# Kernel optimization log

Hardware: AMD Instinct MI355X
Metric: run time of the kernel (lower is better)

## Reference

```python
import jax, jax.numpy as jnp
import numpy as np

V, E, H, L, S, B, FE = 50257, 768, 12, 4, 1024, 2, 4
HD = E // H
EPS = 1e-5


def setup_inputs() -> dict:
    key = jax.random.key(0)
    ks = jax.random.split(key, 16)
    def n(k, shape, scale=0.02):
        return jax.random.normal(k, shape, jnp.float32) * scale
    x = jax.random.randint(ks[0], (B, S), 0, V)
    mask = jnp.tril(jnp.ones((S, S), jnp.int32))[None, None]  # (1,1,S,S) causal
    return {
        "x": x,
        "mask": mask,
        "embed_W": n(ks[1], (V, E)),
        "pos_embed": n(ks[2], (1, S, E)),
        "fc_out_W": n(ks[3], (L, E, E)),
        "fc_out_b": jnp.zeros((L, E), jnp.float32),
        "gate_W": n(ks[4], (L, E, E)),
        "gate_b": jnp.zeros((L, E), jnp.float32),
        "ln1_g": jnp.ones((L, E), jnp.float32),
        "ln1_b": jnp.zeros((L, E), jnp.float32),
        "ln2_g": jnp.ones((L, E), jnp.float32),
        "ln2_b": jnp.zeros((L, E), jnp.float32),
        "ff1_W": n(ks[5], (L, E, FE * E)),
        "ff1_b": jnp.zeros((L, FE * E), jnp.float32),
        "ff2_W": n(ks[6], (L, FE * E, E)),
        "ff2_b": jnp.zeros((L, E), jnp.float32),
        "lnf_g": jnp.ones((E,), jnp.float32),
        "lnf_b": jnp.zeros((E,), jnp.float32),
        "head_W": n(ks[7], (E, V)),
    }


def _layernorm(y, g, b):
    m = jnp.mean(y, -1, keepdims=True)
    v = jnp.mean((y - m) ** 2, -1, keepdims=True)
    return (y - m) * jax.lax.rsqrt(v + EPS) * g + b


def reference(x, mask, embed_W, pos_embed, fc_out_W, fc_out_b, gate_W, gate_b,
              ln1_g, ln1_b, ln2_g, ln2_b, ff1_W, ff1_b, ff2_W, ff2_b,
              lnf_g, lnf_b, head_W):
    h = embed_W[x] + pos_embed[:, :x.shape[1], :]  # (B,S,E)
    scale = 1.0 / np.sqrt(HD)
    for i in range(L):
        # NOTE: source never applies the q/k/v Linear layers; heads are split directly.
        q = h.reshape(B, S, H, HD).transpose(0, 2, 1, 3)  # (B,H,S,HD)
        energy = jnp.einsum('bhqd,bhkd->bhqk', q, q)
        energy = jnp.where(mask == 0, jnp.float32(-1e20), energy)
        attn = jax.nn.softmax(energy * scale, axis=-1)
        o = jnp.einsum('bhqk,bhkd->bhqd', attn, q)
        o = o.transpose(0, 2, 1, 3).reshape(B, S, E)
        o = o @ fc_out_W[i] + fc_out_b[i]
        gate = jax.nn.sigmoid(jnp.mean(h, 1, keepdims=True) @ gate_W[i] + gate_b[i])
        h = _layernorm(gate * o + h, ln1_g[i], ln1_b[i])
        ff = jax.nn.gelu(h @ ff1_W[i] + ff1_b[i], approximate=False) @ ff2_W[i] + ff2_b[i]
        h = _layernorm(ff + h, ln2_g[i], ln2_b[i])
    h = _layernorm(h, lnf_g, lnf_b)
    logits = h @ head_W  # (B,S,V)
    return logits
```

## Files before the change

kernel.cpp:

```cpp
#include <hip/hip_runtime.h>
#include <hip/hip_bf16.h>

#define V 50257
#define E 768
#define NH 12
#define NL 4
#define SS 1024
#define BB 2
#define FEE 4
#define HD 64
#define EPSL 1e-5f
#define NPADH 50432

typedef __hip_bfloat16 bf16;
typedef __attribute__((ext_vector_type(8))) short short8;
typedef __attribute__((ext_vector_type(4))) float f32x4;

#define GLD_SRC(p) (const __attribute__((address_space(1))) void*)(p)
#define GLD_DST(p) (__attribute__((address_space(3))) void*)(p)

__global__ __launch_bounds__(256) void embed_kernel(const int* __restrict__ x, const float* __restrict__ eW,
                                                    const float* __restrict__ pos, float* __restrict__ h){
  size_t i = (size_t)blockIdx.x*256 + threadIdx.x;
  if (i >= (size_t)BB*SS*E) return;
  int e = (int)(i % E);
  size_t bs = i / E;
  int s = (int)(bs % SS);
  int tok = x[bs];
  h[i] = eW[(size_t)tok*E + e] + pos[(size_t)s*E + e];
}

__global__ __launch_bounds__(256) void cvt_attn(const float* __restrict__ h, bf16* __restrict__ hb,
                                                bf16* __restrict__ vT){
  __shared__ float t[64][65];
  int bid = blockIdx.x;
  int st = bid & 15, hh = (bid >> 4) % NH, b = bid / (16*NH);
  int s0 = st*64;
  int c = threadIdx.x & 63, rr = threadIdx.x >> 6;
  #pragma unroll
  for (int i = 0; i < 16; ++i){
    int r = rr*16 + i;
    float v = h[(size_t)(b*SS + s0 + r)*E + hh*HD + c];
    hb[(size_t)(b*SS + s0 + r)*E + hh*HD + c] = __float2bfloat16(v);
    t[r][c] = v;
  }
  __syncthreads();
  #pragma unroll
  for (int i = 0; i < 16; ++i){
    int d = rr*16 + i;
    vT[(size_t)((b*NH + hh)*HD + d)*SS + s0 + c] = __float2bfloat16(t[c][d]);
  }
}

__global__ __launch_bounds__(256) void attn_mfma(const bf16* __restrict__ hb, const bf16* __restrict__ vT,
                                                 bf16* __restrict__ Ab){
  __shared__ short Qs[64*64];
  __shared__ short Ks[128*64];
  __shared__ short Vs[64*128];
  __shared__ short Ps[4][16*128];
  int tid = threadIdx.x, wave = tid >> 6, lane = tid & 63;
  int bid = blockIdx.x;
  int qt = 15 - (bid & 15);
  int hh = (bid >> 4) % NH, b = bid / (16*NH);
  int q0 = qt*64;
  int l15 = lane & 15, l4 = lane >> 4;
  int sw7 = l15 & 7;

  #pragma unroll
  for (int rnd = 0; rnd < 2; ++rnd){
    int o = rnd*256 + tid; int row = o >> 3; int cs = (((o & 7) ^ (row & 7))*8);
    __builtin_amdgcn_global_load_lds(GLD_SRC(hb + ((size_t)(b*SS + q0 + row)*E + hh*HD + cs)),
                                     GLD_DST(Qs + o*8), 16, 0, 0);
  }

  float mrun[4], lrun[4];
  #pragma unroll
  for (int j = 0; j < 4; ++j){ mrun[j] = -1e30f; lrun[j] = 0.f; }
  f32x4 acco[4] = {};

  int nkt = (qt >> 1) + 1;
  for (int kt = 0; kt < nkt; ++kt){
    int k0 = kt*128;
    __syncthreads();
    #pragma unroll
    for (int rnd = 0; rnd < 4; ++rnd){
      int o = rnd*256 + tid; int row = o >> 3; int cs = (((o & 7) ^ (row & 7))*8);
      __builtin_amdgcn_global_load_lds(GLD_SRC(hb + ((size_t)(b*SS + k0 + row)*E + hh*HD + cs)),
                                       GLD_DST(Ks + o*8), 16, 0, 0);
    }
    #pragma unroll
    for (int rnd = 0; rnd < 4; ++rnd){
      int o = rnd*256 + tid; int row = o >> 4; int cs = (((o & 15) ^ (row & 15))*8);
      __builtin_amdgcn_global_load_lds(GLD_SRC(vT + ((size_t)((b*NH + hh)*HD + row)*SS + k0 + cs)),
                                       GLD_DST(Vs + o*8), 16, 0, 0);
    }
    __syncthreads();

    f32x4 s[8] = {};
    __builtin_amdgcn_s_setprio(1);
    #pragma unroll
    for (int kk = 0; kk < 2; ++kk){
      int slot = kk*4 + l4;
      short8 af = *(const short8*)&Qs[(wave*16 + l15)*64 + ((slot ^ sw7)*8)];
      #pragma unroll
      for (int n = 0; n < 8; ++n){
        short8 bf8 = *(const short8*)&Ks[(n*16 + l15)*64 + ((slot ^ sw7)*8)];
        s[n] = __builtin_amdgcn_mfma_f32_16x16x32_bf16(af, bf8, s[n], 0, 0, 0);
      }
    }
    __builtin_amdgcn_s_setprio(0);

    bool diag = (kt == nkt - 1);
    #pragma unroll
    for (int j = 0; j < 4; ++j){
      int qg = q0 + wave*16 + l4*4 + j;
      float tmax = -1e30f;
      #pragma unroll
      for (int n = 0; n < 8; ++n){
        float v = s[n][j]*0.125f;
        if (diag && (k0 + n*16 + l15) > qg) v = -1e30f;
        s[n][j] = v; tmax = fmaxf(tmax, v);
      }
      tmax = fmaxf(tmax, __shfl_xor(tmax, 1, 64));
      tmax = fmaxf(tmax, __shfl_xor(tmax, 2, 64));
      tmax = fmaxf(tmax, __shfl_xor(tmax, 4, 64));
      tmax = fmaxf(tmax, __shfl_xor(tmax, 8, 64));
      float mnew = fmaxf(mrun[j], tmax);
      float alpha = __expf(mrun[j] - mnew);
      float rsum = 0.f;
      #pragma unroll
      for (int n = 0; n < 8; ++n){
        float p = __expf(s[n][j] - mnew);
        s[n][j] = p; rsum += p;
      }
      rsum += __shfl_xor(rsum, 1, 64);
      rsum += __shfl_xor(rsum, 2, 64);
      rsum += __shfl_xor(rsum, 4, 64);
      rsum += __shfl_xor(rsum, 8, 64);
      lrun[j] = lrun[j]*alpha + rsum;
      mrun[j] = mnew;
      #pragma unroll
      for (int n = 0; n < 4; ++n) acco[n][j] *= alpha;
      int prow = l4*4 + j;
      #pragma unroll
      for (int n = 0; n < 8; ++n){
        bf16 hv = __float2bfloat16(s[n][j]);
        int slot = (n*2 + (l15 >> 3)) ^ prow;
        Ps[wave][prow*128 + slot*8 + (l15 & 7)] = __builtin_bit_cast(short, hv);
      }
    }
    __syncthreads();

    __builtin_amdgcn_s_setprio(1);
    #pragma unroll
    for (int kk = 0; kk < 4; ++kk){
      int slot = kk*4 + l4;
      short8 pa = *(const short8*)&Ps[wave][l15*128 + ((slot ^ l15)*8)];
      #pragma unroll
      for (int n = 0; n < 4; ++n){
        short8 vb = *(const short8*)&Vs[(n*16 + l15)*128 + ((slot ^ l15)*8)];
        acco[n] = __builtin_amdgcn_mfma_f32_16x16x32_bf16(pa, vb, acco[n], 0, 0, 0);
      }
    }
    __builtin_amdgcn_s_setprio(0);
  }

  #pragma unroll
  for (int j = 0; j < 4; ++j){
    float inv = 1.f / lrun[j];
    int qg = q0 + wave*16 + l4*4 + j;
    #pragma unroll
    for (int n = 0; n < 4; ++n){
      Ab[(size_t)(b*SS + qg)*E + hh*HD + n*16 + l15] = __float2bfloat16(acco[n][j]*inv);
    }
  }
}

__global__ __launch_bounds__(256) void hmean1_kernel(const float* __restrict__ h, float* __restrict__ ph){
  int bid = blockIdx.x;
  int ec = bid % 3, tc = (bid/3) & 15, b = bid / 48;
  int e = ec*256 + threadIdx.x;
  float s = 0.f;
  #pragma unroll 8
  for (int t = tc*64; t < tc*64 + 64; ++t) s += h[((size_t)b*SS + t)*E + e];
  ph[((size_t)b*16 + tc)*E + e] = s;
}

__global__ __launch_bounds__(256) void gate1_kernel(const float* __restrict__ ph, const float* __restrict__ gW,
                                                    float* __restrict__ pg){
  int bid = blockIdx.x;
  int ec = bid % 3, kc = (bid/3) & 3, b = bid / 12;
  int nn = ec*256 + threadIdx.x;
  __shared__ float hms[192];
  if (threadIdx.x < 192){
    int k = kc*192 + threadIdx.x;
    float s = 0.f;
    #pragma unroll
    for (int tc = 0; tc < 16; ++tc) s += ph[((size_t)b*16 + tc)*E + k];
    hms[threadIdx.x] = s * (1.0f/SS);
  }
  __syncthreads();
  float acc = 0.f;
  #pragma unroll 8
  for (int j = 0; j < 192; ++j) acc += hms[j] * gW[(size_t)(kc*192 + j)*E + nn];
  pg[((size_t)b*4 + kc)*E + nn] = acc;
}

__global__ __launch_bounds__(256) void wcvt_kernel(const float* __restrict__ W, bf16* __restrict__ Wt,
                                                   int K, int N, int Npad){
  int l = blockIdx.z;
  W  += (size_t)l*K*N;
  Wt += (size_t)l*Npad*K;
  __shared__ float t[32][33];
  int n0 = blockIdx.x*32, k0 = blockIdx.y*32;
  int tx = threadIdx.x & 31, ty8 = threadIdx.x >> 5;
  #pragma unroll
  for (int i = 0; i < 4; ++i){
    int k = k0 + ty8 + i*8, n = n0 + tx;
    t[ty8 + i*8][tx] = (k < K && n < N) ? W[(size_t)k*N + n] : 0.f;
  }
  __syncthreads();
  #pragma unroll
  for (int i = 0; i < 4; ++i){
    int n = n0 + ty8 + i*8, k = k0 + tx;
    if (n < Npad && k < K) Wt[(size_t)n*K + k] = __float2bfloat16(t[tx][ty8 + i*8]);
  }
}

template<int EPI>
__global__ __launch_bounds__(256) void mfma_gemm(const bf16* __restrict__ A, const bf16* __restrict__ Bt,
                                                 const float* __restrict__ bias, void* __restrict__ Cv,
                                                 int M, int N, int Kslice, int Ktot){
  __shared__ short As[2][128*64];
  __shared__ short Bs[2][128*64];
  int tid = threadIdx.x;
  int wave = tid >> 6, lane = tid & 63;
  int wr = wave >> 1, wc = wave & 1;
  int l15 = lane & 15, l4 = lane >> 4;
  int sw7 = l15 & 7;
  int n0 = blockIdx.x * 128, m0 = blockIdx.y * 128;
  size_t koff = (size_t)blockIdx.z * Kslice;
  f32x4 acc[4][4] = {};
  int srow = tid >> 3;
  int sj = tid & 7;
  const int nks = Kslice >> 6;

  #define STAGE128(bsel, kt) do {                                              \
    int kb = (kt)*64;                                                          \
    _Pragma("unroll")                                                          \
    for (int iss = 0; iss < 4; ++iss){                                         \
      int r = srow + iss*32;                                                   \
      int cs = ((sj ^ (r & 7))*8);                                             \
      __builtin_amdgcn_global_load_lds(GLD_SRC(A + (size_t)(m0 + r)*Ktot + koff + kb + cs),  \
                                       GLD_DST(&As[bsel][r*64 + sj*8]), 16, 0, 0);           \
      __builtin_amdgcn_global_load_lds(GLD_SRC(Bt + (size_t)(n0 + r)*Ktot + koff + kb + cs), \
                                       GLD_DST(&Bs[bsel][r*64 + sj*8]), 16, 0, 0);           \
    }                                                                          \
  } while(0)

  STAGE128(0, 0);
  __syncthreads();
  for (int kt = 0; kt < nks; ++kt){
    int cur = kt & 1;
    if (kt + 1 < nks) STAGE128(cur ^ 1, kt + 1);
    __builtin_amdgcn_s_setprio(1);
    #pragma unroll
    for (int kk = 0; kk < 2; ++kk){
      int slot = kk*4 + l4;
      short8 af[4], bfr[4];
      #pragma unroll
      for (int m = 0; m < 4; ++m)
        af[m] = *(const short8*)&As[cur][(wr*64 + m*16 + l15)*64 + ((slot ^ sw7)*8)];
      #pragma unroll
      for (int n = 0; n < 4; ++n)
        bfr[n] = *(const short8*)&Bs[cur][(wc*64 + n*16 + l15)*64 + ((slot ^ sw7)*8)];
      #pragma unroll
      for (int m = 0; m < 4; ++m)
        #pragma unroll
        for (int n = 0; n < 4; ++n)
          acc[m][n] = __builtin_amdgcn_mfma_f32_16x16x32_bf16(af[m], bfr[n], acc[m][n], 0, 0, 0);
    }
    __builtin_amdgcn_s_setprio(0);
    __syncthreads();
  }
  #undef STAGE128

  float* Cf = (float*)Cv + (size_t)blockIdx.z * M * N;
  int lrow = l4*4;
  #pragma unroll
  for (int m = 0; m < 4; ++m){
    int row = m0 + wr*64 + m*16 + lrow;
    #pragma unroll
    for (int n = 0; n < 4; ++n){
      int col = n0 + wc*64 + n*16 + l15;
      if (col >= N) continue;
      #pragma unroll
      for (int j = 0; j < 4; ++j){
        float v = acc[m][n][j];
        if (EPI == 3){
          v += bias[col];
          v = 0.5f*v*(1.0f + erff(v*0.70710678f));
          ((bf16*)Cv)[(size_t)(row + j)*N + col] = __float2bfloat16(v);
        } else {
          Cf[(size_t)(row + j)*N + col] = v;
        }
      }
    }
  }
}

__global__ __launch_bounds__(512, 2) void gemm256(const bf16* __restrict__ A, const bf16* __restrict__ Bt,
                                                  float* __restrict__ C, int M, int N, int K, int MT){
  __shared__ short As[2][256*64];
  __shared__ short Bs[2][256*64];
  int tid = threadIdx.x;
  int wave = tid >> 6, lane = tid & 63;
  int wr = wave >> 2, wc = wave & 3;
  int l15 = lane & 15, l4 = lane >> 4;
  int sw7 = l15 & 7;

  int lid = blockIdx.x;
  int cpx = gridDim.x >> 3;
  int wg = (lid & 7)*cpx + (lid >> 3);
  int m0 = (wg % MT)*256, n0 = (wg / MT)*256;

  int srow = tid >> 3;
  int sj = tid & 7;
  const int nks = K >> 6;

  #define STAGE256(bsel, kt) do {                                             \
    int kb = (kt)*64;                                                         \
    _Pragma("unroll")                                                         \
    for (int rnd = 0; rnd < 4; ++rnd){                                        \
      int r = rnd*64 + srow;                                                  \
      int cs = ((sj ^ (r & 7))*8);                                            \
      __builtin_amdgcn_global_load_lds(GLD_SRC(A + (size_t)(m0 + r)*K + kb + cs),   \
                                       GLD_DST(&As[bsel][r*64 + sj*8]), 16, 0, 0);  \
      __builtin_amdgcn_global_load_lds(GLD_SRC(Bt + (size_t)(n0 + r)*K + kb + cs),  \
                                       GLD_DST(&Bs[bsel][r*64 + sj*8]), 16, 0, 0);  \
    }                                                                         \
  } while(0)

  f32x4 acc[8][4] = {};
  STAGE256(0, 0);
  __syncthreads();
  for (int kt = 0; kt < nks; ++kt){
    int cur = kt & 1;
    if (kt + 1 < nks) STAGE256(cur ^ 1, kt + 1);
    __builtin_amdgcn_s_setprio(1);
    #pragma unroll
    for (int kk = 0; kk < 2; ++kk){
      int slot = kk*4 + l4;
      short8 af[8], bfr[4];
      #pragma unroll
      for (int m = 0; m < 8; ++m)
        af[m] = *(const short8*)&As[cur][(wr*128 + m*16 + l15)*64 + ((slot ^ sw7)*8)];
      #pragma unroll
      for (int n = 0; n < 4; ++n)
        bfr[n] = *(const short8*)&Bs[cur][(wc*64 + n*16 + l15)*64 + ((slot ^ sw7)*8)];
      #pragma unroll
      for (int m = 0; m < 8; ++m)
        #pragma unroll
        for (int n = 0; n < 4; ++n)
          acc[m][n] = __builtin_amdgcn_mfma_f32_16x16x32_bf16(af[m], bfr[n], acc[m][n], 0, 0, 0);
    }
    __builtin_amdgcn_s_setprio(0);
    __syncthreads();
  }
  #undef STAGE256

  int lrow = l4*4;
  #pragma unroll
  for (int m = 0; m < 8; ++m){
    int row = m0 + wr*128 + m*16 + lrow;
    #pragma unroll
    for (int n = 0; n < 4; ++n){
      int col = n0 + wc*64 + n*16 + l15;
      if (col >= N) continue;
      #pragma unroll
      for (int j = 0; j < 4; ++j)
        C[(size_t)(row + j)*N + col] = acc[m][n][j];
    }
  }
}

__global__ __launch_bounds__(256) void ln_kernel(const float* __restrict__ parts, int np,
                                                 const float* __restrict__ bias,
                                                 const float* __restrict__ resid,
                                                 const float* __restrict__ pg, const float* __restrict__ gb,
                                                 const float* __restrict__ g, const float* __restrict__ bta,
                                                 float* __restrict__ out, bf16* __restrict__ outb){
  const size_t PS = (size_t)BB*SS*E;
  int row = blockIdx.x;
  int b = row >> 10;
  int tid = threadIdx.x;
  __shared__ float sred[4];
  float y[3];
  float lsum = 0.f;
  #pragma unroll
  for (int i = 0; i < 3; ++i){
    int e = tid + i*256;
    float v = bias ? bias[e] : 0.f;
    for (int p = 0; p < np; ++p) v += parts[(size_t)p*PS + (size_t)row*E + e];
    if (pg){
      float ga = pg[(size_t)(b*4+0)*E + e] + pg[(size_t)(b*4+1)*E + e]
               + pg[(size_t)(b*4+2)*E + e] + pg[(size_t)(b*4+3)*E + e] + gb[e];
      v *= 1.0f / (1.0f + __expf(-ga));
    }
    if (resid) v += resid[(size_t)row*E + e];
    y[i] = v; lsum += v;
  }
  for (int off = 32; off > 0; off >>= 1) lsum += __shfl_down(lsum, off, 64);
  int wid = tid >> 6, lane = tid & 63;
  if (lane == 0) sred[wid] = lsum;
  __syncthreads();
  float mean = (sred[0]+sred[1]+sred[2]+sred[3]) * (1.0f/E);
  __syncthreads();
  float lvar = 0.f;
  #pragma unroll
  for (int i = 0; i < 3; ++i){ float d = y[i]-mean; lvar += d*d; }
  for (int off = 32; off > 0; off >>= 1) lvar += __shfl_down(lvar, off, 64);
  if (lane == 0) sred[wid] = lvar;
  __syncthreads();
  float rstd = rsqrtf((sred[0]+sred[1]+sred[2]+sred[3]) * (1.0f/E) + EPSL);
  __syncthreads();
  #pragma unroll
  for (int i = 0; i < 3; ++i){
    int e = tid + i*256;
    float r = (y[i]-mean)*rstd*g[e] + bta[e];
    out[(size_t)row*E + e] = r;
    if (outb) outb[(size_t)row*E + e] = __float2bfloat16(r);
  }
}

extern "C" void kernel_launch(void* const* d_in, const int* in_sizes, int n_in,
                              void* d_out, int out_size, void* d_ws, size_t ws_size,
                              hipStream_t stream) {
  const int*   x      = (const int*)  d_in[0];
  const float* embedW = (const float*)d_in[2];
  const float* pos    = (const float*)d_in[3];
  const float* fcW    = (const float*)d_in[4];
  const float* fcB    = (const float*)d_in[5];
  const float* gW     = (const float*)d_in[6];
  const float* gB     = (const float*)d_in[7];
  const float* ln1g   = (const float*)d_in[8];
  const float* ln1b   = (const float*)d_in[9];
  const float* ln2g   = (const float*)d_in[10];
  const float* ln2b   = (const float*)d_in[11];
  const float* f1W    = (const float*)d_in[12];
  const float* f1B    = (const float*)d_in[13];
  const float* f2W    = (const float*)d_in[14];
  const float* f2B    = (const float*)d_in[15];
  const float* lnfg   = (const float*)d_in[16];
  const float* lnfb   = (const float*)d_in[17];
  const float* headW  = (const float*)d_in[18];
  float* out = (float*)d_out;

  const size_t BSE = (size_t)BB*SS*E;
  float* h    = (float*)d_ws;
  float* o    = h   + BSE;
  float* tmp  = o   + BSE;
  float* ph   = tmp + 2*BSE;
  float* pg   = ph  + (size_t)BB*16*E;
  bf16* abA   = (bf16*)(pg + (size_t)BB*4*E);
  bf16* abF   = abA + BSE;
  bf16* WfcT  = abF + BSE*FEE;
  bf16* Wf1T  = WfcT + (size_t)NL*E*E;
  bf16* Wf2T  = Wf1T + (size_t)NL*FEE*E*E;
  bf16* WheadT= Wf2T + (size_t)NL*FEE*E*E;
  bf16* hb    = (bf16*)o;
  bf16* vT    = hb + BSE;

  const int rows = BB*SS;

  embed_kernel<<<(int)((BSE + 255)/256), 256, 0, stream>>>(x, embedW, pos, h);

  { dim3 g(E/32, E/32, NL);        wcvt_kernel<<<g, 256, 0, stream>>>(fcW, WfcT, E, E, E); }
  { dim3 g((FEE*E)/32, E/32, NL);  wcvt_kernel<<<g, 256, 0, stream>>>(f1W, Wf1T, E, FEE*E, FEE*E); }
  { dim3 g(E/32, (FEE*E)/32, NL);  wcvt_kernel<<<g, 256, 0, stream>>>(f2W, Wf2T, FEE*E, E, E); }
  { dim3 g(NPADH/32, E/32, 1);     wcvt_kernel<<<g, 256, 0, stream>>>(headW, WheadT, E, V, NPADH); }

  for (int l = 0; l < NL; ++l){
    size_t oEE = (size_t)l*E*E, oE = (size_t)l*E, oFb = (size_t)l*FEE*E;

    hmean1_kernel<<<BB*16*3, 256, 0, stream>>>(h, ph);
    gate1_kernel<<<BB*4*3, 256, 0, stream>>>(ph, gW + oEE, pg);

    cvt_attn<<<BB*NH*16, 256, 0, stream>>>(h, hb, vT);
    attn_mfma<<<BB*NH*16, 256, 0, stream>>>(hb, vT, abA);

    { dim3 g(E/128, rows/128, 2);
      mfma_gemm<0><<<g, 256, 0, stream>>>(abA, WfcT + oEE, nullptr, tmp, rows, E, E/2, E); }

    ln_kernel<<<rows, 256, 0, stream>>>(tmp, 2, fcB + oE, h, pg, gB + oE,
                                        ln1g + oE, ln1b + oE, h, abA);

    { dim3 g((FEE*E)/128, rows/128, 1);
      mfma_gemm<3><<<g, 256, 0, stream>>>(abA, Wf1T + (size_t)l*FEE*E*E, f1B + oFb, abF, rows, FEE*E, E, E); }

    { dim3 g(E/128, rows/128, 2);
      mfma_gemm<0><<<g, 256, 0, stream>>>(abF, Wf2T + (size_t)l*FEE*E*E, nullptr, tmp, rows, E, FEE*E/2, FEE*E); }

    ln_kernel<<<rows, 256, 0, stream>>>(tmp, 2, f2B + oE, h, nullptr, nullptr,
                                        ln2g + oE, ln2b + oE, h, nullptr);
  }

  ln_kernel<<<rows, 256, 0, stream>>>(h, 1, nullptr, nullptr, nullptr, nullptr,
                                      lnfg, lnfb, tmp, abA);
  {
    gemm256<<<(rows/256)*(NPADH/256), 512, 0, stream>>>(abA, WheadT, out, rows, V, E, rows/256);
  }
}
```

Measured before the change: 1.030 ms.

## Reuse 128-tile MFMA GEMM for LM head with XCD mapping and finer waits

Removes the dedicated 256x256-tile, 512-thread head GEMM. The vocab projection now runs on the shared 128x128 MFMA GEMM, which gains an optional XCD-aware block remapping. The shared GEMM's pipeline replaces full __syncthreads with explicit s_waitcnt vmcnt(8) plus raw barriers, so only the current stage's loads are awaited while the prefetch stays in flight. It also requests two blocks per CU via launch bounds. Smaller head tiles raise block count and occupancy but lower per-tile data reuse, so global/L2 traffic for the large vocab GEMM goes up.

```diff
diff --git a/kernel.cpp b/kernel.cpp
--- a/kernel.cpp
+++ b/kernel.cpp
@@ -227,10 +227,10 @@
   }
 }
 
-template<int EPI>
-__global__ __launch_bounds__(256) void mfma_gemm(const bf16* __restrict__ A, const bf16* __restrict__ Bt,
-                                                 const float* __restrict__ bias, void* __restrict__ Cv,
-                                                 int M, int N, int Kslice, int Ktot){
+template<int EPI, bool XCDMAP>
+__global__ __launch_bounds__(256, 2) void mfma_gemm(const bf16* __restrict__ A, const bf16* __restrict__ Bt,
+                                                    const float* __restrict__ bias, void* __restrict__ Cv,
+                                                    int M, int N, int Kslice, int Ktot, int MTm){
   __shared__ short As[2][128*64];
   __shared__ short Bs[2][128*64];
   int tid = threadIdx.x;
@@ -238,7 +238,15 @@
   int wr = wave >> 1, wc = wave & 1;
   int l15 = lane & 15, l4 = lane >> 4;
   int sw7 = l15 & 7;
-  int n0 = blockIdx.x * 128, m0 = blockIdx.y * 128;
+  int m0, n0;
+  if (XCDMAP){
+    int lid = blockIdx.x;
+    int q = gridDim.x >> 3;
+    int wg = (lid & 7)*q + (lid >> 3);
+    m0 = (wg % MTm)*128; n0 = (wg / MTm)*128;
+  } else {
+    n0 = blockIdx.x * 128; m0 = blockIdx.y * 128;
+  }
   size_t koff = (size_t)blockIdx.z * Kslice;
   f32x4 acc[4][4] = {};
   int srow = tid >> 3;
@@ -259,10 +267,16 @@
   } while(0)
 
   STAGE128(0, 0);
-  __syncthreads();
   for (int kt = 0; kt < nks; ++kt){
     int cur = kt & 1;
-    if (kt + 1 < nks) STAGE128(cur ^ 1, kt + 1);
+    if (kt + 1 < nks){
+      STAGE128(cur ^ 1, kt + 1);
+      asm volatile("s_waitcnt vmcnt(8)" ::: "memory");
+    } else {
+      asm volatile("s_waitcnt vmcnt(0)" ::: "memory");
+    }
+    __builtin_amdgcn_s_barrier();
+    __builtin_amdgcn_sched_barrier(0);
     __builtin_amdgcn_s_setprio(1);
     #pragma unroll
     for (int kk = 0; kk < 2; ++kk){
@@ -281,7 +295,8 @@
           acc[m][n] = __builtin_amdgcn_mfma_f32_16x16x32_bf16(af[m], bfr[n], acc[m][n], 0, 0, 0);
     }
     __builtin_amdgcn_s_setprio(0);
-    __syncthreads();
+    __builtin_amdgcn_s_barrier();
+    __builtin_amdgcn_sched_barrier(0);
   }
   #undef STAGE128
 
@@ -305,81 +320,6 @@
           Cf[(size_t)(row + j)*N + col] = v;
         }
       }
-    }
-  }
-}
-
-__global__ __launch_bounds__(512, 2) void gemm256(const bf16* __restrict__ A, const bf16* __restrict__ Bt,
-                                                  float* __restrict__ C, int M, int N, int K, int MT){
-  __shared__ short As[2][256*64];
-  __shared__ short Bs[2][256*64];
-  int tid = threadIdx.x;
-  int wave = tid >> 6, lane = tid & 63;
-  int wr = wave >> 2, wc = wave & 3;
-  int l15 = lane & 15, l4 = lane >> 4;
-  int sw7 = l15 & 7;
-
-  int lid = blockIdx.x;
-  int cpx = gridDim.x >> 3;
-  int wg = (lid & 7)*cpx + (lid >> 3);
-  int m0 = (wg % MT)*256, n0 = (wg / MT)*256;
-
-  int srow = tid >> 3;
-  int sj = tid & 7;
-  const int nks = K >> 6;
-
-  #define STAGE256(bsel, kt) do {                                             \
-    int kb = (kt)*64;                                                         \
-    _Pragma("unroll")                                                         \
-    for (int rnd = 0; rnd < 4; ++rnd){                                        \
-      int r = rnd*64 + srow;                                                  \
-      int cs = ((sj ^ (r & 7))*8);                                            \
-      __builtin_amdgcn_global_load_lds(GLD_SRC(A + (size_t)(m0 + r)*K + kb + cs),   \
-                                       GLD_DST(&As[bsel][r*64 + sj*8]), 16, 0, 0);  \
-      __builtin_amdgcn_global_load_lds(GLD_SRC(Bt + (size_t)(n0 + r)*K + kb + cs),  \
-                                       GLD_DST(&Bs[bsel][r*64 + sj*8]), 16, 0, 0);  \
-    }                                                                         \
-  } while(0)
-
-  f32x4 acc[8][4] = {};
-  STAGE256(0, 0);
-  __syncthreads();
-  for (int kt = 0; kt < nks; ++kt){
-    int cur = kt & 1;
-    if (kt + 1 < nks) STAGE256(cur ^ 1, kt + 1);
-    __builtin_amdgcn_s_setprio(1);
-    #pragma unroll
-    for (int kk = 0; kk < 2; ++kk){
-      int slot = kk*4 + l4;
-      short8 af[8], bfr[4];
-      #pragma unroll
-      for (int m = 0; m < 8; ++m)
-        af[m] = *(const short8*)&As[cur][(wr*128 + m*16 + l15)*64 + ((slot ^ sw7)*8)];
-      #pragma unroll
-      for (int n = 0; n < 4; ++n)
-        bfr[n] = *(const short8*)&Bs[cur][(wc*64 + n*16 + l15)*64 + ((slot ^ sw7)*8)];
-      #pragma unroll
-      for (int m = 0; m < 8; ++m)
-        #pragma unroll
-        for (int n = 0; n < 4; ++n)
-          acc[m][n] = __builtin_amdgcn_mfma_f32_16x16x32_bf16(af[m], bfr[n], acc[m][n], 0, 0, 0);
-    }
-    __builtin_amdgcn_s_setprio(0);
-    __syncthreads();
-  }
-  #undef STAGE256
-
-  int lrow = l4*4;
-  #pragma unroll
-  for (int m = 0; m < 8; ++m){
-    int row = m0 + wr*128 + m*16 + lrow;
-    #pragma unroll
-    for (int n = 0; n < 4; ++n){
-      int col = n0 + wc*64 + n*16 + l15;
-      if (col >= N) continue;
-      #pragma unroll
-      for (int j = 0; j < 4; ++j)
-        C[(size_t)(row + j)*N + col] = acc[m][n][j];
     }
   }
 }
@@ -490,16 +430,16 @@
     attn_mfma<<<BB*NH*16, 256, 0, stream>>>(hb, vT, abA);
 
     { dim3 g(E/128, rows/128, 2);
-      mfma_gemm<0><<<g, 256, 0, stream>>>(abA, WfcT + oEE, nullptr, tmp, rows, E, E/2, E); }
+      mfma_gemm<0,false><<<g, 256, 0, stream>>>(abA, WfcT + oEE, nullptr, tmp, rows, E, E/2, E, 0); }
 
     ln_kernel<<<rows, 256, 0, stream>>>(tmp, 2, fcB + oE, h, pg, gB + oE,
                                         ln1g + oE, ln1b + oE, h, abA);
 
     { dim3 g((FEE*E)/128, rows/128, 1);
-      mfma_gemm<3><<<g, 256, 0, stream>>>(abA, Wf1T + (size_t)l*FEE*E*E, f1B + oFb, abF, rows, FEE*E, E, E); }
+      mfma_gemm<3,false><<<g, 256, 0, stream>>>(abA, Wf1T + (size_t)l*FEE*E*E, f1B + oFb, abF, rows, FEE*E, E, E, 0); }
 
     { dim3 g(E/128, rows/128, 2);
-      mfma_gemm<0><<<g, 256, 0, stream>>>(abF, Wf2T + (size_t)l*FEE*E*E, nullptr, tmp, rows, E, FEE*E/2, FEE*E); }
+      mfma_gemm<0,false><<<g, 256, 0, stream>>>(abF, Wf2T + (size_t)l*FEE*E*E, nullptr, tmp, rows, E, FEE*E/2, FEE*E, 0); }
 
     ln_kernel<<<rows, 256, 0, stream>>>(tmp, 2, f2B + oE, h, nullptr, nullptr,
                                         ln2g + oE, ln2b + oE, h, nullptr);
@@ -508,6 +448,7 @@
   ln_kernel<<<rows, 256, 0, stream>>>(h, 1, nullptr, nullptr, nullptr, nullptr,
                                       lnfg, lnfb, tmp, abA);
   {
-    gemm256<<<(rows/256)*(NPADH/256), 512, 0, stream>>>(abA, WheadT, out, rows, V, E, rows/256);
-  }
-}
+    mfma_gemm<0,true><<<(rows/128)*(NPADH/128), 256, 0, stream>>>(
+        abA, WheadT, nullptr, out, rows, V, E, E, rows/128);
+  }
+}
```

Result: slower. 1.053 ms (+2.3%).

## Fuse bf16 activation conversion upstream and use fine-grained vmcnt waits in GEMMs

Applied to the files above, without the earlier changes.

The embedding and second layernorm kernels now write the bf16 copy of the hidden state directly, so cvt_attn only transposes bf16 data instead of reading fp32 and converting. The GEMM main loops replace __syncthreads with explicit vmcnt waits that keep the next stage's async global-to-LDS loads in flight while waiting only for the current stage, plus raw barriers. The mfma_gemm launch bounds request two blocks per CU. The risks are correctness if the vmcnt count is wrong and register pressure from the occupancy hint.

```diff
diff --git a/kernel.cpp b/kernel.cpp
--- a/kernel.cpp
+++ b/kernel.cpp
@@ -20,19 +20,21 @@
 #define GLD_DST(p) (__attribute__((address_space(3))) void*)(p)
 
 __global__ __launch_bounds__(256) void embed_kernel(const int* __restrict__ x, const float* __restrict__ eW,
-                                                    const float* __restrict__ pos, float* __restrict__ h){
+                                                    const float* __restrict__ pos, float* __restrict__ h,
+                                                    bf16* __restrict__ hb){
   size_t i = (size_t)blockIdx.x*256 + threadIdx.x;
   if (i >= (size_t)BB*SS*E) return;
   int e = (int)(i % E);
   size_t bs = i / E;
   int s = (int)(bs % SS);
   int tok = x[bs];
-  h[i] = eW[(size_t)tok*E + e] + pos[(size_t)s*E + e];
-}
-
-__global__ __launch_bounds__(256) void cvt_attn(const float* __restrict__ h, bf16* __restrict__ hb,
-                                                bf16* __restrict__ vT){
-  __shared__ float t[64][65];
+  float v = eW[(size_t)tok*E + e] + pos[(size_t)s*E + e];
+  h[i] = v;
+  hb[i] = __float2bfloat16(v);
+}
+
+__global__ __launch_bounds__(256) void cvt_attn(const bf16* __restrict__ hb, bf16* __restrict__ vT){
+  __shared__ short t[64][65];
   int bid = blockIdx.x;
   int st = bid & 15, hh = (bid >> 4) % NH, b = bid / (16*NH);
   int s0 = st*64;
@@ -40,15 +42,13 @@
   #pragma unroll
   for (int i = 0; i < 16; ++i){
     int r = rr*16 + i;
-    float v = h[(size_t)(b*SS + s0 + r)*E + hh*HD + c];
-    hb[(size_t)(b*SS + s0 + r)*E + hh*HD + c] = __float2bfloat16(v);
-    t[r][c] = v;
+    t[r][c] = __builtin_bit_cast(short, hb[(size_t)(b*SS + s0 + r)*E + hh*HD + c]);
   }
   __syncthreads();
   #pragma unroll
   for (int i = 0; i < 16; ++i){
     int d = rr*16 + i;
-    vT[(size_t)((b*NH + hh)*HD + d)*SS + s0 + c] = __float2bfloat16(t[c][d]);
+    vT[(size_t)((b*NH + hh)*HD + d)*SS + s0 + c] = __builtin_bit_cast(bf16, t[c][d]);
   }
 }
 
@@ -228,9 +228,9 @@
 }
 
 template<int EPI>
-__global__ __launch_bounds__(256) void mfma_gemm(const bf16* __restrict__ A, const bf16* __restrict__ Bt,
-                                                 const float* __restrict__ bias, void* __restrict__ Cv,
-                                                 int M, int N, int Kslice, int Ktot){
+__global__ __launch_bounds__(256, 2) void mfma_gemm(const bf16* __restrict__ A, const bf16* __restrict__ Bt,
+                                                    const float* __restrict__ bias, void* __restrict__ Cv,
+                                                    int M, int N, int Kslice, int Ktot){
   __shared__ short As[2][128*64];
   __shared__ short Bs[2][128*64];
   int tid = threadIdx.x;
@@ -259,10 +259,16 @@
   } while(0)
 
   STAGE128(0, 0);
-  __syncthreads();
   for (int kt = 0; kt < nks; ++kt){
     int cur = kt & 1;
-    if (kt + 1 < nks) STAGE128(cur ^ 1, kt + 1);
+    if (kt + 1 < nks){
+      STAGE128(cur ^ 1, kt + 1);
+      asm volatile("s_waitcnt vmcnt(8)" ::: "memory");
+    } else {
+      asm volatile("s_waitcnt vmcnt(0)" ::: "memory");
+    }
+    __builtin_amdgcn_s_barrier();
+    __builtin_amdgcn_sched_barrier(0);
     __builtin_amdgcn_s_setprio(1);
     #pragma unroll
     for (int kk = 0; kk < 2; ++kk){
@@ -281,7 +287,8 @@
           acc[m][n] = __builtin_amdgcn_mfma_f32_16x16x32_bf16(af[m], bfr[n], acc[m][n], 0, 0, 0);
     }
     __builtin_amdgcn_s_setprio(0);
-    __syncthreads();
+    __builtin_amdgcn_s_barrier();
+    __builtin_amdgcn_sched_barrier(0);
   }
   #undef STAGE128
 
@@ -343,10 +350,16 @@
 
   f32x4 acc[8][4] = {};
   STAGE256(0, 0);
-  __syncthreads();
   for (int kt = 0; kt < nks; ++kt){
     int cur = kt & 1;
-    if (kt + 1 < nks) STAGE256(cur ^ 1, kt + 1);
+    if (kt + 1 < nks){
+      STAGE256(cur ^ 1, kt + 1);
+      asm volatile("s_waitcnt vmcnt(8)" ::: "memory");
+    } else {
+      asm volatile("s_waitcnt vmcnt(0)" ::: "memory");
+    }
+    __builtin_amdgcn_s_barrier();
+    __builtin_amdgcn_sched_barrier(0);
     __builtin_amdgcn_s_setprio(1);
     #pragma unroll
     for (int kk = 0; kk < 2; ++kk){
@@ -365,7 +378,8 @@
           acc[m][n] = __builtin_amdgcn_mfma_f32_16x16x32_bf16(af[m], bfr[n], acc[m][n], 0, 0, 0);
     }
     __builtin_amdgcn_s_setprio(0);
-    __syncthreads();
+    __builtin_amdgcn_s_barrier();
+    __builtin_amdgcn_sched_barrier(0);
   }
   #undef STAGE256
 
@@ -473,7 +487,7 @@
 
   const int rows = BB*SS;
 
-  embed_kernel<<<(int)((BSE + 255)/256), 256, 0, stream>>>(x, embedW, pos, h);
+  embed_kernel<<<(int)((BSE + 255)/256), 256, 0, stream>>>(x, embedW, pos, h, hb);
 
   { dim3 g(E/32, E/32, NL);        wcvt_kernel<<<g, 256, 0, stream>>>(fcW, WfcT, E, E, E); }
   { dim3 g((FEE*E)/32, E/32, NL);  wcvt_kernel<<<g, 256, 0, stream>>>(f1W, Wf1T, E, FEE*E, FEE*E); }
@@ -486,7 +500,7 @@
     hmean1_kernel<<<BB*16*3, 256, 0, stream>>>(h, ph);
     gate1_kernel<<<BB*4*3, 256, 0, stream>>>(ph, gW + oEE, pg);
 
-    cvt_attn<<<BB*NH*16, 256, 0, stream>>>(h, hb, vT);
+    cvt_attn<<<BB*NH*16, 256, 0, stream>>>(hb, vT);
     attn_mfma<<<BB*NH*16, 256, 0, stream>>>(hb, vT, abA);
 
     { dim3 g(E/128, rows/128, 2);
@@ -502,7 +516,7 @@
       mfma_gemm<0><<<g, 256, 0, stream>>>(abF, Wf2T + (size_t)l*FEE*E*E, nullptr, tmp, rows, E, FEE*E/2, FEE*E); }
 
     ln_kernel<<<rows, 256, 0, stream>>>(tmp, 2, f2B + oE, h, nullptr, nullptr,
-                                        ln2g + oE, ln2b + oE, h, nullptr);
+                                        ln2g + oE, ln2b + oE, h, hb);
   }
 
   ln_kernel<<<rows, 256, 0, stream>>>(h, 1, nullptr, nullptr, nullptr, nullptr,
```

Result: no change. 1.022 ms (-0.7%).
